# Kernel optimization log

Hardware: AMD Instinct MI355X
Metric: run time of the kernel (lower is better)

The kernel has to match this reference:

```python
import jax, jax.numpy as jnp
import numpy as np
import math

D_MODEL = 2048
NUM_HEADS = 16
QUERY_GROUPS = 4
HEAD_DIM = D_MODEL // NUM_HEADS  # 128
B, T = 2, 2048


def setup_inputs() -> dict:
    key = jax.random.key(0)
    ks = jax.random.split(key, 9)
    s = 0.02
    return {
        "x": jax.random.normal(ks[0], (B, T, D_MODEL), dtype=jnp.float32),
        "Wq": jax.random.normal(ks[1], (D_MODEL, NUM_HEADS * HEAD_DIM), dtype=jnp.float32) * s,
        "bq": jnp.zeros((NUM_HEADS * HEAD_DIM,), dtype=jnp.float32),
        "Wk": jax.random.normal(ks[2], (D_MODEL, QUERY_GROUPS * HEAD_DIM), dtype=jnp.float32) * s,
        "bk": jnp.zeros((QUERY_GROUPS * HEAD_DIM,), dtype=jnp.float32),
        "Wv": jax.random.normal(ks[3], (D_MODEL, QUERY_GROUPS * HEAD_DIM), dtype=jnp.float32) * s,
        "bv": jnp.zeros((QUERY_GROUPS * HEAD_DIM,), dtype=jnp.float32),
        "Wo": jax.random.normal(ks[4], (D_MODEL, D_MODEL), dtype=jnp.float32) * s,
        "bo": jnp.zeros((D_MODEL,), dtype=jnp.float32),
    }


def reference(x, Wq, bq, Wk, bk, Wv, bv, Wo, bo):
    Bb, Tt, Dd = x.shape
    G, H, hd = QUERY_GROUPS, NUM_HEADS, HEAD_DIM
    m = H // G  # heads per group
    # projections
    q = (x @ Wq + bq).reshape(Bb, Tt, G, m, hd)   # [B,T,G,m,hd]
    k = (x @ Wk + bk).reshape(Bb, Tt, G, hd)      # [B,T,G,hd]
    v = (x @ Wv + bv).reshape(Bb, Tt, G, hd)
    # scores with native group broadcast (no explicit K/V expansion)
    scores = jnp.einsum('btgmd,bsgd->bgmts', q, k) / math.sqrt(hd)  # [B,G,m,T,T]
    p = jax.nn.softmax(scores, axis=-1)
    out = jnp.einsum('bgmts,bsgd->btgmd', p, v).reshape(Bb, Tt, Dd)
    # output projection (dropout is identity in eval / p=0)
    return out @ Wo + bo
```

## Files before the change

kernel.cpp:

```cpp
#include <hip/hip_runtime.h>

#define D_MODEL 2048
#define T_SEQ   2048
#define NBATCH  2
#define NH      16
#define NG      4
#define HD      128
#define NQKV    3072

typedef short bf16x8 __attribute__((ext_vector_type(8)));
typedef float f32x4  __attribute__((ext_vector_type(4)));
typedef float f32x16 __attribute__((ext_vector_type(16)));
typedef short s16x4  __attribute__((ext_vector_type(4)));
typedef unsigned u32x4 __attribute__((ext_vector_type(4)));

__device__ __forceinline__ short f2bf(float f) {
  union { float f; unsigned u; } v; v.f = f;
  unsigned r = v.u + 0x7fffu + ((v.u >> 16) & 1u);
  return (short)(r >> 16);
}

__device__ __forceinline__ float bf2f(short s) {
  union { unsigned u; float f; } v; v.u = ((unsigned)(unsigned short)s) << 16;
  return v.f;
}

__device__ __forceinline__ float fast_exp2(float x) {
#if __has_builtin(__builtin_amdgcn_exp2f)
  return __builtin_amdgcn_exp2f(x);
#else
  return __expf(x * 0.6931471805599453f);
#endif
}

__device__ __forceinline__ unsigned cvt_pk_bf16(float a, float b) {
  unsigned r;
  asm("v_cvt_pk_bf16_f32 %0, %1, %2" : "=v"(r) : "v"(a), "v"(b));
  return r;
}

__device__ __forceinline__ void permlane32_swap(unsigned &a, unsigned &b) {
  asm("v_permlane32_swap_b32 %0, %1" : "+v"(a), "+v"(b));
}

__device__ __forceinline__ void gload16(const void* g, void* l) {
  __builtin_amdgcn_global_load_lds(
      (const __attribute__((address_space(1))) void*)g,
      (__attribute__((address_space(3))) void*)l, 16, 0, 0);
}

__global__ __launch_bounds__(256) void convert_x_kernel(
    const float* __restrict__ x, short* __restrict__ o, int n) {
  int i = (blockIdx.x * 256 + threadIdx.x) * 4;
  if (i >= n) return;
  float4 v = *(const float4*)(x + i);
  s16x4 s;
  s[0] = f2bf(v.x); s[1] = f2bf(v.y); s[2] = f2bf(v.z); s[3] = f2bf(v.w);
  *(s16x4*)(o + i) = s;
}

__global__ __launch_bounds__(256) void wtrans_kernel(
    const float* __restrict__ W, short* __restrict__ dst,
    int K, int N, int rowOff, int dstStride) {
  __shared__ float t[32][33];
  int tx = threadIdx.x & 31, ty = threadIdx.x >> 5;
  int kb = blockIdx.x * 32, nb = blockIdx.y * 32;
#pragma unroll
  for (int i = 0; i < 4; ++i)
    t[ty + 8*i][tx] = W[(long)(kb + ty + 8*i) * N + nb + tx];
  __syncthreads();
#pragma unroll
  for (int i = 0; i < 4; ++i)
    dst[(long)(rowOff + nb + ty + 8*i) * dstStride + kb + tx] = f2bf(t[tx][ty + 8*i]);
}

__global__ __launch_bounds__(256) void vtrans_kernel(
    const short* __restrict__ qkv, short* __restrict__ vt) {
  __shared__ short t[32][33];
  int bg = blockIdx.z; int b = bg >> 2, g = bg & 3;
  int sb = blockIdx.x * 32, db = blockIdx.y * 32;
  int tx = threadIdx.x & 31, ty = threadIdx.x >> 5;
  const short* src = qkv + (long)(b * T_SEQ) * NQKV + D_MODEL + NG * HD + g * HD;
#pragma unroll
  for (int i = 0; i < 4; ++i)
    t[ty + 8*i][tx] = src[(long)(sb + ty + 8*i) * NQKV + db + tx];
  __syncthreads();
  short* dst = vt + ((long)bg * HD + db) * T_SEQ + sb;
#pragma unroll
  for (int i = 0; i < 4; ++i)
    dst[(long)(ty + 8*i) * T_SEQ + tx] = t[tx][ty + 8*i];
}

__global__ __launch_bounds__(256) void gemm_kernel(
    const short* __restrict__ A, const short* __restrict__ BT,
    const float* __restrict__ b0, const float* __restrict__ b1, const float* __restrict__ b2,
    void* __restrict__ Cout, int M, int N, int K, int mode) {
  __shared__ __align__(16) short As[128 * 64];
  __shared__ __align__(16) short Bs[128 * 64];
  const int tid = threadIdx.x;
  const int w = tid >> 6, lane = tid & 63;
  const int l15 = lane & 15, quad = lane >> 4;
  const int wr = w & 1, wc = w >> 1;
  const int nb = blockIdx.x, mb = blockIdx.y;
  const short* Ab = A + (long)mb * 128 * K;
  const short* Bb = BT + (long)nb * 128 * K;

  f32x4 acc[4][4];
#pragma unroll
  for (int i = 0; i < 4; ++i)
#pragma unroll
    for (int j = 0; j < 4; ++j) acc[i][j] = 0.0f;

  for (int k0 = 0; k0 < K; k0 += 64) {
    __syncthreads();
#pragma unroll
    for (int t = 0; t < 4; ++t) {
      int chunk = w * 256 + t * 64 + lane;
      int r = chunk >> 3, c = chunk & 7;
      int gc = c ^ (r & 7);
      gload16(Ab + (long)r * K + k0 + gc * 8, As + (w * 256 + t * 64) * 8);
      gload16(Bb + (long)r * K + k0 + gc * 8, Bs + (w * 256 + t * 64) * 8);
    }
    __syncthreads();
#pragma unroll
    for (int ks = 0; ks < 2; ++ks) {
      bf16x8 af[4], bfr[4];
#pragma unroll
      for (int i = 0; i < 4; ++i) {
        int r = wr * 64 + i * 16 + l15;
        af[i] = *(const bf16x8*)(As + r * 64 + (((ks * 4 + quad) ^ (r & 7)) * 8));
      }
#pragma unroll
      for (int j = 0; j < 4; ++j) {
        int r = wc * 64 + j * 16 + l15;
        bfr[j] = *(const bf16x8*)(Bs + r * 64 + (((ks * 4 + quad) ^ (r & 7)) * 8));
      }
#pragma unroll
      for (int i = 0; i < 4; ++i)
#pragma unroll
        for (int j = 0; j < 4; ++j)
          acc[i][j] = __builtin_amdgcn_mfma_f32_16x16x32_bf16(af[i], bfr[j], acc[i][j], 0, 0, 0);
    }
  }

  float biasv[4];
#pragma unroll
  for (int j = 0; j < 4; ++j) {
    int col = nb * 128 + wc * 64 + j * 16 + l15;
    float bv;
    if (mode == 0) {
      if (col < 2048)      bv = b0[col];
      else if (col < 2560) bv = b1[col - 2048];
      else                 bv = b2[col - 2560];
    } else bv = b0[col];
    biasv[j] = bv;
  }
  if (mode == 0) {
    short* C = (short*)Cout;
#pragma unroll
    for (int i = 0; i < 4; ++i)
#pragma unroll
      for (int j = 0; j < 4; ++j)
#pragma unroll
        for (int r = 0; r < 4; ++r) {
          int row = mb * 128 + wr * 64 + i * 16 + quad * 4 + r;
          int col = nb * 128 + wc * 64 + j * 16 + l15;
          C[(long)row * N + col] = f2bf(acc[i][j][r] + biasv[j]);
        }
  } else {
    float* C = (float*)Cout;
#pragma unroll
    for (int i = 0; i < 4; ++i)
#pragma unroll
      for (int j = 0; j < 4; ++j)
#pragma unroll
        for (int r = 0; r < 4; ++r) {
          int row = mb * 128 + wr * 64 + i * 16 + quad * 4 + r;
          int col = nb * 128 + wc * 64 + j * 16 + l15;
          C[(long)row * N + col] = acc[i][j][r] + biasv[j];
        }
  }
}

__global__ __launch_bounds__(256, 2) void attn_kernel(
    const short* __restrict__ qkv, const short* __restrict__ vt,
    short* __restrict__ aout) {
  __shared__ __align__(16) short smem[32768];

  const int tid = threadIdx.x;
  const int w = tid >> 6, lane = tid & 63;
  const int l31 = lane & 31, hi = lane >> 5;
  const int qt = blockIdx.x, h = blockIdx.y, b = blockIdx.z;
  const int g = h >> 2;
  const short* qbase = qkv + (long)(b * T_SEQ + qt * 128) * NQKV + h * HD;
  const short* kbase = qkv + (long)(b * T_SEQ) * NQKV + D_MODEL + g * HD;
  const short* vbase = vt + (long)(b * NG + g) * HD * T_SEQ;
  const float QSCALE = 0.08838834764831845f * 1.4426950408889634f;

  int kroff[4], vroff[4], dst[4];
#pragma unroll
  for (int t = 0; t < 4; ++t) {
    int chunk = w * 256 + t * 64 + lane;
    { int r = chunk >> 4, c = chunk & 15, gc = c ^ (r & 15);
      kroff[t] = r * NQKV + gc * 8; }
    { int r = chunk >> 3, c = chunk & 7, gc = c ^ (r & 7);
      vroff[t] = r * T_SEQ + gc * 8; }
    dst[t] = chunk * 8;
  }

  bf16x8 qfrag[8];
  {
    const short* qrow = qbase + (long)(w * 32 + l31) * NQKV + hi * 8;
#pragma unroll
    for (int ks = 0; ks < 8; ++ks) {
      bf16x8 v = *(const bf16x8*)(qrow + ks * 16);
#pragma unroll
      for (int e = 0; e < 8; ++e) v[e] = f2bf(bf2f(v[e]) * QSCALE);
      qfrag[ks] = v;
    }
  }

#pragma unroll
  for (int t = 0; t < 4; ++t) {
    gload16(kbase + kroff[t], smem + dst[t]);
    gload16(vbase + vroff[t], smem + 8192 + dst[t]);
  }

  f32x16 oaccT[4];
#pragma unroll
  for (int i = 0; i < 4; ++i) oaccT[i] = 0.0f;
  float lpart[4] = {0.f, 0.f, 0.f, 0.f};

  __syncthreads();

  int cur = 0;
  bf16x8 kpre[4], vpre[4];
  for (int st = 0; st < T_SEQ / 64; ++st) {
    const bool pf = (st + 1 < T_SEQ / 64);
    short* Ks = smem + cur * 16384;
    short* Vs = Ks + 8192;
    if (pf) {
      const short* kb2 = kbase + (long)(st + 1) * 64 * NQKV;
      const short* vb2 = vbase + (st + 1) * 64;
#pragma unroll
      for (int t = 0; t < 4; ++t) {
        kpre[t] = *(const bf16x8*)(kb2 + kroff[t]);
        vpre[t] = *(const bf16x8*)(vb2 + vroff[t]);
      }
    }

    f32x16 sacc[2][2];
    sacc[0][0] = 0.0f; sacc[0][1] = 0.0f; sacc[1][0] = 0.0f; sacc[1][1] = 0.0f;
    __builtin_amdgcn_s_setprio(1);
#pragma unroll
    for (int ks = 0; ks < 8; ++ks) {
#pragma unroll
      for (int sb = 0; sb < 2; ++sb) {
        int srow = sb * 32 + l31;
        bf16x8 a = *(const bf16x8*)(Ks + srow * 128 + (((ks * 2 + hi) ^ (srow & 15)) * 8));
        sacc[sb][ks & 1] = __builtin_amdgcn_mfma_f32_32x32x16_bf16(a, qfrag[ks], sacc[sb][ks & 1], 0, 0, 0);
      }
    }
    __builtin_amdgcn_s_setprio(0);

    float p0[16], p1[16];
#pragma unroll
    for (int r = 0; r < 16; ++r) p0[r] = fast_exp2(sacc[0][0][r] + sacc[0][1][r]);
#pragma unroll
    for (int r = 0; r < 16; ++r) p1[r] = fast_exp2(sacc[1][0][r] + sacc[1][1][r]);
#pragma unroll
    for (int r = 0; r < 16; ++r) lpart[r & 3] += p0[r] + p1[r];

    __builtin_amdgcn_s_setprio(1);
#pragma unroll
    for (int k2 = 0; k2 < 4; ++k2) {
      const float* pp = (k2 & 2) ? p1 : p0;
      const int bo = (k2 & 1) * 8;
      unsigned Pa = cvt_pk_bf16(pp[bo + 0], pp[bo + 1]);
      unsigned Pb = cvt_pk_bf16(pp[bo + 2], pp[bo + 3]);
      unsigned Pc = cvt_pk_bf16(pp[bo + 4], pp[bo + 5]);
      unsigned Pd = cvt_pk_bf16(pp[bo + 6], pp[bo + 7]);
      permlane32_swap(Pa, Pc);
      permlane32_swap(Pb, Pd);
      u32x4 pu; pu[0] = Pa; pu[1] = Pb; pu[2] = Pc; pu[3] = Pd;
      bf16x8 pfr = __builtin_bit_cast(bf16x8, pu);
#pragma unroll
      for (int db = 0; db < 4; ++db) {
        int drow = db * 32 + l31;
        bf16x8 a = *(const bf16x8*)(Vs + drow * 64 + (((k2 * 2 + hi) ^ (drow & 7)) * 8));
        oaccT[db] = __builtin_amdgcn_mfma_f32_32x32x16_bf16(a, pfr, oaccT[db], 0, 0, 0);
      }
    }
    __builtin_amdgcn_s_setprio(0);

    if (pf) {
      short* Kn = smem + (cur ^ 1) * 16384;
      short* Vn = Kn + 8192;
#pragma unroll
      for (int t = 0; t < 4; ++t) {
        *(bf16x8*)(Kn + dst[t]) = kpre[t];
        *(bf16x8*)(Vn + dst[t]) = vpre[t];
      }
    }
    __syncthreads();
    cur ^= 1;
  }

  float lsum = (lpart[0] + lpart[1]) + (lpart[2] + lpart[3]);
  float lfull = lsum + __shfl_xor(lsum, 32);
  float inv = 1.0f / lfull;

  short* Osm = smem;
  const int qrl = w * 32 + l31;
#pragma unroll
  for (int db = 0; db < 4; ++db)
#pragma unroll
    for (int r = 0; r < 16; ++r) {
      int dloc = (r & 3) + 8 * (r >> 2) + 4 * hi;
      int d = db * 32 + dloc;
      int c = d >> 3;
      Osm[qrl * 128 + ((c ^ (qrl & 15)) * 8) + (d & 7)] = f2bf(oaccT[db][r] * inv);
    }
  __syncthreads();

  short* obase = aout + (long)(b * T_SEQ + qt * 128) * D_MODEL + h * HD;
  const int row = tid >> 1, ch = tid & 1;
#pragma unroll
  for (int j = 0; j < 8; ++j) {
    int c2 = ch * 8 + j;
    bf16x8 v = *(const bf16x8*)(Osm + row * 128 + ((c2 ^ (row & 15)) * 8));
    *(bf16x8*)(obase + (long)row * D_MODEL + c2 * 8) = v;
  }
}

extern "C" void kernel_launch(void* const* d_in, const int* in_sizes, int n_in,
                              void* d_out, int out_size, void* d_ws, size_t ws_size,
                              hipStream_t stream) {
  const float* x  = (const float*)d_in[0];
  const float* Wq = (const float*)d_in[1];
  const float* bq = (const float*)d_in[2];
  const float* Wk = (const float*)d_in[3];
  const float* bk = (const float*)d_in[4];
  const float* Wv = (const float*)d_in[5];
  const float* bv = (const float*)d_in[6];
  const float* Wo = (const float*)d_in[7];
  const float* bo = (const float*)d_in[8];

  const long NTOK = (long)NBATCH * T_SEQ;
  short* xb    = (short*)d_ws;
  short* wqkvT = xb + NTOK * D_MODEL;
  short* woT   = wqkvT + (long)NQKV * D_MODEL;
  short* qkvb  = woT + (long)D_MODEL * D_MODEL;
  short* vtb   = qkvb + NTOK * NQKV;
  short* attnb = vtb + (long)NBATCH * NG * HD * T_SEQ;

  int nX = (int)(NTOK * D_MODEL);
  convert_x_kernel<<<nX / (256 * 4), 256, 0, stream>>>(x, xb, nX);
  wtrans_kernel<<<dim3(D_MODEL / 32, D_MODEL / 32), 256, 0, stream>>>(Wq, wqkvT, D_MODEL, D_MODEL, 0, D_MODEL);
  wtrans_kernel<<<dim3(D_MODEL / 32, 512 / 32), 256, 0, stream>>>(Wk, wqkvT, D_MODEL, 512, 2048, D_MODEL);
  wtrans_kernel<<<dim3(D_MODEL / 32, 512 / 32), 256, 0, stream>>>(Wv, wqkvT, D_MODEL, 512, 2560, D_MODEL);
  wtrans_kernel<<<dim3(D_MODEL / 32, D_MODEL / 32), 256, 0, stream>>>(Wo, woT, D_MODEL, D_MODEL, 0, D_MODEL);

  gemm_kernel<<<dim3(NQKV / 128, NTOK / 128), 256, 0, stream>>>(
      xb, wqkvT, bq, bk, bv, (void*)qkvb, (int)NTOK, NQKV, D_MODEL, 0);

  vtrans_kernel<<<dim3(T_SEQ / 32, HD / 32, NBATCH * NG), 256, 0, stream>>>(qkvb, vtb);

  attn_kernel<<<dim3(T_SEQ / 128, NH, NBATCH), 256, 0, stream>>>(qkvb, vtb, attnb);

  gemm_kernel<<<dim3(D_MODEL / 128, NTOK / 128), 256, 0, stream>>>(
      attnb, woT, bo, bo, bo, (void*)d_out, (int)NTOK, D_MODEL, D_MODEL, 1);
}
```

Baseline: 334.2 us.

## Use 256-row double-buffered GEMM tiles with 512 threads for projections

Replaces the 128x128 single-buffered GEMM with a templated kernel using 256-row tiles, 512 threads, and double-buffered LDS so the next K-slice loads while MFMAs run on the current one. QKV uses 256x256 tiles and the output projection uses 256x128 tiles. It also raises wave priority around the MFMA block and precomputes load offsets. The aim is more reuse per tile and hidden global-load latency, at the cost of much more LDS and registers per block. The QKV grid also shrinks to 192 blocks, which may underfill the GPU's compute units.

```diff
diff --git a/kernel.cpp b/kernel.cpp
--- a/kernel.cpp
+++ b/kernel.cpp
@@ -91,92 +91,128 @@
     dst[(long)(ty + 8*i) * T_SEQ + tx] = t[tx][ty + 8*i];
 }
 
-__global__ __launch_bounds__(256) void gemm_kernel(
+template <int BN, int MODE>
+__global__ __launch_bounds__(512, 2) void gemm256_kernel(
     const short* __restrict__ A, const short* __restrict__ BT,
     const float* __restrict__ b0, const float* __restrict__ b1, const float* __restrict__ b2,
-    void* __restrict__ Cout, int M, int N, int K, int mode) {
-  __shared__ __align__(16) short As[128 * 64];
-  __shared__ __align__(16) short Bs[128 * 64];
+    void* __restrict__ Cout, int M, int N, int K) {
+  constexpr int BM = 256, BK = 64;
+  constexpr int NFR = BN / 64;
+  constexpr int ASZ = BM * BK;
+  constexpr int BSZ = BN * BK;
+  constexpr int ACH = (ASZ * 2 / 16) / 512;
+  constexpr int BCH = (BSZ * 2 / 16) / 512;
+  __shared__ __align__(16) short smem[(ASZ + BSZ) * 2];
+
   const int tid = threadIdx.x;
   const int w = tid >> 6, lane = tid & 63;
   const int l15 = lane & 15, quad = lane >> 4;
   const int wr = w & 1, wc = w >> 1;
   const int nb = blockIdx.x, mb = blockIdx.y;
-  const short* Ab = A + (long)mb * 128 * K;
-  const short* Bb = BT + (long)nb * 128 * K;
-
-  f32x4 acc[4][4];
-#pragma unroll
-  for (int i = 0; i < 4; ++i)
-#pragma unroll
-    for (int j = 0; j < 4; ++j) acc[i][j] = 0.0f;
-
-  for (int k0 = 0; k0 < K; k0 += 64) {
-    __syncthreads();
-#pragma unroll
-    for (int t = 0; t < 4; ++t) {
-      int chunk = w * 256 + t * 64 + lane;
-      int r = chunk >> 3, c = chunk & 7;
-      int gc = c ^ (r & 7);
-      gload16(Ab + (long)r * K + k0 + gc * 8, As + (w * 256 + t * 64) * 8);
-      gload16(Bb + (long)r * K + k0 + gc * 8, Bs + (w * 256 + t * 64) * 8);
-    }
-    __syncthreads();
+  const short* Ab = A + (long)mb * BM * K;
+  const short* Bb = BT + (long)nb * BN * K;
+
+  f32x4 acc[8][NFR];
+#pragma unroll
+  for (int i = 0; i < 8; ++i)
+#pragma unroll
+    for (int j = 0; j < NFR; ++j) acc[i][j] = 0.0f;
+
+  int aoff[ACH], boff[BCH];
+#pragma unroll
+  for (int i = 0; i < ACH; ++i) {
+    int chunk = i * 512 + tid;
+    int r = chunk >> 3, c = chunk & 7, gc = c ^ (r & 7);
+    aoff[i] = r * K + gc * 8;
+  }
+#pragma unroll
+  for (int i = 0; i < BCH; ++i) {
+    int chunk = i * 512 + tid;
+    int r = chunk >> 3, c = chunk & 7, gc = c ^ (r & 7);
+    boff[i] = r * K + gc * 8;
+  }
+
+#pragma unroll
+  for (int i = 0; i < ACH; ++i) gload16(Ab + aoff[i], smem + (i * 512 + tid) * 8);
+#pragma unroll
+  for (int i = 0; i < BCH; ++i) gload16(Bb + boff[i], smem + ASZ + (i * 512 + tid) * 8);
+
+  const int NT = K / BK;
+  int cur = 0;
+  for (int t = 0; t < NT; ++t) {
+    asm volatile("s_waitcnt vmcnt(0)" ::: "memory");
+    __builtin_amdgcn_s_barrier();
+    asm volatile("" ::: "memory");
+    if (t + 1 < NT) {
+      const int k0n = (t + 1) * BK;
+      short* An = smem + (cur ^ 1) * (ASZ + BSZ);
+      short* Bn = An + ASZ;
+#pragma unroll
+      for (int i = 0; i < ACH; ++i) gload16(Ab + k0n + aoff[i], An + (i * 512 + tid) * 8);
+#pragma unroll
+      for (int i = 0; i < BCH; ++i) gload16(Bb + k0n + boff[i], Bn + (i * 512 + tid) * 8);
+    }
+    __builtin_amdgcn_sched_barrier(0);
+    const short* As = smem + cur * (ASZ + BSZ);
+    const short* Bs = As + ASZ;
 #pragma unroll
     for (int ks = 0; ks < 2; ++ks) {
-      bf16x8 af[4], bfr[4];
-#pragma unroll
-      for (int i = 0; i < 4; ++i) {
-        int r = wr * 64 + i * 16 + l15;
+      bf16x8 af[8], bfr[NFR];
+#pragma unroll
+      for (int i = 0; i < 8; ++i) {
+        int r = wr * 128 + i * 16 + l15;
         af[i] = *(const bf16x8*)(As + r * 64 + (((ks * 4 + quad) ^ (r & 7)) * 8));
       }
 #pragma unroll
-      for (int j = 0; j < 4; ++j) {
-        int r = wc * 64 + j * 16 + l15;
+      for (int j = 0; j < NFR; ++j) {
+        int r = wc * (NFR * 16) + j * 16 + l15;
         bfr[j] = *(const bf16x8*)(Bs + r * 64 + (((ks * 4 + quad) ^ (r & 7)) * 8));
       }
-#pragma unroll
-      for (int i = 0; i < 4; ++i)
-#pragma unroll
-        for (int j = 0; j < 4; ++j)
+      __builtin_amdgcn_s_setprio(1);
+#pragma unroll
+      for (int i = 0; i < 8; ++i)
+#pragma unroll
+        for (int j = 0; j < NFR; ++j)
           acc[i][j] = __builtin_amdgcn_mfma_f32_16x16x32_bf16(af[i], bfr[j], acc[i][j], 0, 0, 0);
-    }
-  }
-
-  float biasv[4];
-#pragma unroll
-  for (int j = 0; j < 4; ++j) {
-    int col = nb * 128 + wc * 64 + j * 16 + l15;
+      __builtin_amdgcn_s_setprio(0);
+    }
+    cur ^= 1;
+  }
+
+  float biasv[NFR];
+#pragma unroll
+  for (int j = 0; j < NFR; ++j) {
+    int col = nb * BN + wc * (NFR * 16) + j * 16 + l15;
     float bv;
-    if (mode == 0) {
+    if (MODE == 0) {
       if (col < 2048)      bv = b0[col];
       else if (col < 2560) bv = b1[col - 2048];
       else                 bv = b2[col - 2560];
     } else bv = b0[col];
     biasv[j] = bv;
   }
-  if (mode == 0) {
+  if (MODE == 0) {
     short* C = (short*)Cout;
 #pragma unroll
-    for (int i = 0; i < 4; ++i)
-#pragma unroll
-      for (int j = 0; j < 4; ++j)
+    for (int i = 0; i < 8; ++i)
+#pragma unroll
+      for (int j = 0; j < NFR; ++j)
 #pragma unroll
         for (int r = 0; r < 4; ++r) {
-          int row = mb * 128 + wr * 64 + i * 16 + quad * 4 + r;
-          int col = nb * 128 + wc * 64 + j * 16 + l15;
+          int row = mb * BM + wr * 128 + i * 16 + quad * 4 + r;
+          int col = nb * BN + wc * (NFR * 16) + j * 16 + l15;
           C[(long)row * N + col] = f2bf(acc[i][j][r] + biasv[j]);
         }
   } else {
     float* C = (float*)Cout;
 #pragma unroll
-    for (int i = 0; i < 4; ++i)
-#pragma unroll
-      for (int j = 0; j < 4; ++j)
+    for (int i = 0; i < 8; ++i)
+#pragma unroll
+      for (int j = 0; j < NFR; ++j)
 #pragma unroll
         for (int r = 0; r < 4; ++r) {
-          int row = mb * 128 + wr * 64 + i * 16 + quad * 4 + r;
-          int col = nb * 128 + wc * 64 + j * 16 + l15;
+          int row = mb * BM + wr * 128 + i * 16 + quad * 4 + r;
+          int col = nb * BN + wc * (NFR * 16) + j * 16 + l15;
           C[(long)row * N + col] = acc[i][j][r] + biasv[j];
         }
   }
@@ -361,13 +397,13 @@
   wtrans_kernel<<<dim3(D_MODEL / 32, 512 / 32), 256, 0, stream>>>(Wv, wqkvT, D_MODEL, 512, 2560, D_MODEL);
   wtrans_kernel<<<dim3(D_MODEL / 32, D_MODEL / 32), 256, 0, stream>>>(Wo, woT, D_MODEL, D_MODEL, 0, D_MODEL);
 
-  gemm_kernel<<<dim3(NQKV / 128, NTOK / 128), 256, 0, stream>>>(
-      xb, wqkvT, bq, bk, bv, (void*)qkvb, (int)NTOK, NQKV, D_MODEL, 0);
+  gemm256_kernel<256, 0><<<dim3(NQKV / 256, NTOK / 256), 512, 0, stream>>>(
+      xb, wqkvT, bq, bk, bv, (void*)qkvb, (int)NTOK, NQKV, D_MODEL);
 
   vtrans_kernel<<<dim3(T_SEQ / 32, HD / 32, NBATCH * NG), 256, 0, stream>>>(qkvb, vtb);
 
   attn_kernel<<<dim3(T_SEQ / 128, NH, NBATCH), 256, 0, stream>>>(qkvb, vtb, attnb);
 
-  gemm_kernel<<<dim3(D_MODEL / 128, NTOK / 128), 256, 0, stream>>>(
-      attnb, woT, bo, bo, bo, (void*)d_out, (int)NTOK, D_MODEL, D_MODEL, 1);
-}
+  gemm256_kernel<128, 1><<<dim3(D_MODEL / 128, NTOK / 256), 512, 0, stream>>>(
+      attnb, woT, bo, bo, bo, (void*)d_out, (int)NTOK, D_MODEL, D_MODEL);
+}
```

After: 305.7 us. 1.09x faster.
